# Kernel tuning notes

Measured on AMD Instinct MI355X. Metric: run time of the kernel, lower is better.

The kernel has to match this reference:

```python
import jax, jax.numpy as jnp
import numpy as np

NUM_JOINTS = 24
NUM_THETAS = NUM_JOINTS * 3  # 72
NUM_VERTS = 6890
NUM_BETAS = 10
BATCH = 512

SMPL_PARENTS = np.array([0, 0, 0, 0, 1, 2, 3, 4, 5, 6, 7, 8, 9, 9, 9,
                         12, 13, 14, 16, 17, 18, 19, 20, 21], dtype=np.int32)


def setup_inputs() -> dict:
    key = jax.random.key(0)
    ks = jax.random.split(key, 6)
    x = jax.random.normal(ks[0], (BATCH, NUM_THETAS + NUM_BETAS), dtype=jnp.float32) * 0.3
    v_template = jax.random.normal(ks[1], (NUM_VERTS, 3), dtype=jnp.float32) * 0.3
    shapedirs = jax.random.normal(ks[2], (NUM_BETAS, NUM_VERTS * 3), dtype=jnp.float32) * 0.01
    posedirs = jax.random.normal(ks[3], (207, NUM_VERTS * 3), dtype=jnp.float32) * 0.001
    Jr = jax.random.uniform(ks[4], (NUM_VERTS, NUM_JOINTS), dtype=jnp.float32)
    J_regressor = Jr / jnp.sum(Jr, axis=0, keepdims=True)
    W = jax.random.uniform(ks[5], (NUM_VERTS, NUM_JOINTS), dtype=jnp.float32)
    lbs_weights = W / jnp.sum(W, axis=1, keepdims=True)  # rows sum to 1 (skinning weights)
    parents = jnp.asarray(SMPL_PARENTS)
    return {"x": x, "v_template": v_template, "shapedirs": shapedirs,
            "J_regressor": J_regressor, "posedirs": posedirs,
            "lbs_weights": lbs_weights, "parents": parents}


def batch_rodrigues(theta):
    # theta: [N,3] axis-angle -> [N,3,3] rotation matrices
    angle = jnp.linalg.norm(theta + 1e-8, axis=1, keepdims=True)  # [N,1]
    r = theta / angle                                              # [N,3] unit axis
    cos = jnp.cos(angle)[..., None]                                # [N,1,1]
    sin = jnp.sin(angle)[..., None]
    outer = r[:, :, None] * r[:, None, :]                          # [N,3,3]
    rx, ry, rz = r[:, 0], r[:, 1], r[:, 2]
    zero = jnp.zeros_like(rx)
    K = jnp.stack([zero, -rz, ry,
                   rz, zero, -rx,
                   -ry, rx, zero], axis=1).reshape(-1, 3, 3)       # skew-symmetric
    eye = jnp.eye(3, dtype=theta.dtype)
    return cos * eye + (1.0 - cos) * outer + sin * K


def global_rigid_transformation(Rs, J, parents):
    # Rs: [B,24,3,3], J: [B,24,3] -> A: [B,24,4,4]
    B = Rs.shape[0]
    dtype = Rs.dtype
    bottom = jnp.broadcast_to(jnp.array([0, 0, 0, 1], dtype=dtype), (B, 1, 4))

    def make_A(R, t):  # R:[B,3,3], t:[B,3]
        Rt = jnp.concatenate([R, t[:, :, None]], axis=2)  # [B,3,4]
        return jnp.concatenate([Rt, bottom], axis=1)       # [B,4,4]

    parents = np.asarray(parents)
    results = [make_A(Rs[:, 0], J[:, 0])]
    for i in range(1, NUM_JOINTS):
        t_rel = J[:, i] - J[:, parents[i]]
        A_here = make_A(Rs[:, i], t_rel)
        results.append(jnp.matmul(results[parents[i]], A_here))
    results = jnp.stack(results, axis=1)  # [B,24,4,4]

    Js_w0 = jnp.concatenate([J, jnp.zeros((B, NUM_JOINTS, 1), dtype=dtype)], axis=2)  # [B,24,4]
    init_bone = jnp.einsum('bjpq,bjq->bjp', results, Js_w0)                           # [B,24,4]
    A = results - jnp.pad(init_bone[..., None], ((0, 0), (0, 0), (0, 0), (3, 0)))
    return A


def reference(x, v_template, shapedirs, J_regressor, posedirs, lbs_weights, parents):
    B = x.shape[0]
    thetas = x[:, :NUM_THETAS]
    betas = x[:, NUM_THETAS:]

    # shape blendshapes
    v_shaped = (betas @ shapedirs).reshape(B, NUM_VERTS, 3) + v_template  # [B,V,3]

    J = jnp.einsum('bvc,vj->bjc', v_shaped, J_regressor)  # [B,24,3]

    # pose rotations + pose blendshapes
    Rs = batch_rodrigues(thetas.reshape(-1, 3)).reshape(B, NUM_JOINTS, 3, 3)
    pose_feature = (Rs[:, 1:] - jnp.eye(3, dtype=x.dtype)).reshape(B, 207)
    v_posed = (pose_feature @ posedirs).reshape(B, NUM_VERTS, 3) + v_shaped

    # kinematic chain
    A = global_rigid_transformation(Rs, J, parents)  # [B,24,4,4]

    # linear blend skinning
    T = jnp.einsum('vj,bjpq->bvpq', lbs_weights, A)  # [B,V,4,4]
    v_posed_homo = jnp.concatenate(
        [v_posed, jnp.ones((B, NUM_VERTS, 1), dtype=x.dtype)], axis=2)  # [B,V,4]
    verts = jnp.einsum('bvpq,bvq->bvp', T, v_posed_homo)[:, :, :3]
    return verts
```

## Files before the change

### kernel.cpp

```cpp
#include <hip/hip_runtime.h>

#define NUM_JOINTS 24
#define NUM_VERTS  6890
#define NUM_COORDS (NUM_VERTS * 3)
#define NUM_BETAS  10
#define KTOT       217
#define KPAD       224
#define BATCH      512
#define VPAD       6912

#define WS_SJP  0
#define WS_XBF  85536
#define WS_DBF  142880
#define WS_WHBF 2465312
#define WS_AH   2575904
#define WS_AL   2706976

typedef __attribute__((ext_vector_type(8))) short short8;
typedef __attribute__((ext_vector_type(4))) float f32x4;

__device__ inline unsigned short f2bf(float f) {
    union { float f; unsigned u; } c; c.f = f;
    unsigned u = c.u;
    u += 0x7fffu + ((u >> 16) & 1u);
    return (unsigned short)(u >> 16);
}
__device__ inline float bf2f(unsigned short h) {
    union { unsigned u; float f; } c; c.u = ((unsigned)h) << 16;
    return c.f;
}

struct PBShm {
    float Rs[4][24][9];
    float Jl[4][24][3];
    float Rg[4][24][9];
    float tg[4][24][3];
    float As[4][24][12];
};

__global__ __launch_bounds__(256) void k_prep(const float* __restrict__ Jr,
                                              const float* __restrict__ sd,
                                              const float* __restrict__ pd,
                                              const float* __restrict__ vt,
                                              const float* __restrict__ w,
                                              float* __restrict__ ws) {
    __shared__ __align__(16) unsigned char smem[28928];
    const int t   = blockIdx.x;
    const int tid = threadIdx.x;
    unsigned short* whbf = (unsigned short*)(ws + WS_WHBF);
    unsigned short* dbf  = (unsigned short*)(ws + WS_DBF);

    if (t < 27) {
        const int v = t * 256 + tid;
        const bool ok = (v < NUM_VERTS);
        unsigned short row[32];
        #pragma unroll
        for (int j = 0; j < 32; ++j)
            row[j] = f2bf((ok && j < 24) ? w[v * 24 + j] : 0.f);
        #pragma unroll
        for (int i = 0; i < 4; ++i)
            *(float4*)(whbf + (size_t)v * 32 + i * 8) = *(const float4*)(&row[i * 8]);
    } else if (t < 351) {
        unsigned* L = (unsigned*)smem;
        const int c0   = (t - 27) * 64;
        const int lane = tid & 63;
        const int grp  = tid >> 6;
        const int c    = c0 + lane;
        const bool cv  = (c < NUM_COORDS);
        #pragma unroll 4
        for (int i = 0; i < 28; ++i) {
            const int p  = i * 4 + grp;
            const int k0 = 2 * p, k1 = k0 + 1;
            float v0 = 0.f, v1 = 0.f;
            if (cv) {
                v0 = (k0 < 10) ? sd[(size_t)k0 * NUM_COORDS + c]
                   : (k0 < KTOT) ? pd[(size_t)(k0 - 10) * NUM_COORDS + c] : 0.f;
                v1 = (k1 < 10) ? sd[(size_t)k1 * NUM_COORDS + c]
                   : (k1 < KTOT) ? pd[(size_t)(k1 - 10) * NUM_COORDS + c] : 0.f;
            }
            L[lane * 113 + p] = (unsigned)f2bf(v0) | ((unsigned)f2bf(v1) << 16);
        }
        __syncthreads();
        #pragma unroll
        for (int i = 0; i < 7; ++i) {
            const int idx = i * 256 + tid;
            const int row = idx / 28;
            const int q   = idx % 28;
            uint4 val;
            val.x = L[row * 113 + q * 4 + 0];
            val.y = L[row * 113 + q * 4 + 1];
            val.z = L[row * 113 + q * 4 + 2];
            val.w = L[row * 113 + q * 4 + 3];
            *(uint4*)(dbf + (size_t)(c0 + row) * KPAD + q * 8) = val;
        }
    } else {
        float* Jl = (float*)smem;
        float* S  = (float*)smem + 64 * 25;
        const int strip = t - 351;
        const int v0 = strip * 64;
        #pragma unroll
        for (int i = 0; i < 6; ++i) {
            const int idx = i * 256 + tid;
            const int v = idx / 24, j = idx % 24;
            Jl[v * 25 + j] = (v0 + v < NUM_VERTS) ? Jr[(size_t)(v0 + v) * 24 + j] : 0.f;
        }
        #pragma unroll
        for (int i = 0; i < 9; ++i) {
            const int idx = i * 256 + tid;
            if (idx < 33 * 64) {
                const int s = idx / 64, v = idx % 64;
                float val = 0.f;
                if (v0 + v < NUM_VERTS) {
                    if (s < 30) val = sd[(size_t)(s / 3) * NUM_COORDS + (size_t)(v0 + v) * 3 + (s % 3)];
                    else        val = vt[(size_t)(v0 + v) * 3 + (s - 30)];
                }
                S[s * 64 + v] = val;
            }
        }
        __syncthreads();
        float* wsp = ws + WS_SJP + (size_t)strip * 792;
        for (int o = tid; o < 792; o += 256) {
            const int s = o / 24, j = o % 24;
            float sum = 0.f;
            #pragma unroll 8
            for (int v = 0; v < 64; ++v)
                sum += S[s * 64 + v] * Jl[v * 25 + j];
            wsp[o] = sum;
        }
    }
}

__global__ __launch_bounds__(256) void k_pb(const float* __restrict__ x,
                                            const int* __restrict__ parents,
                                            float* __restrict__ ws) {
    __shared__ PBShm P;
    __shared__ float SJf[792];
    unsigned short* xbf = (unsigned short*)(ws + WS_XBF);
    unsigned short* ahi = (unsigned short*)(ws + WS_AH);
    unsigned short* alo = (unsigned short*)(ws + WS_AL);
    const int tid = threadIdx.x;

    {
        const float* wsp = ws + WS_SJP;
        for (int o = tid; o < 792; o += 256) {
            float sum = 0.f;
            for (int s2 = 0; s2 < 108; ++s2)
                sum += wsp[(size_t)s2 * 792 + o];
            SJf[o] = sum;
        }
    }
    __syncthreads();

    const int sub  = tid >> 6;
    const int lane = tid & 63;
    const int b = blockIdx.x * 4 + sub;
    const float* row = x + b * (NUM_BETAS + 72);

    if (lane < 24) {
        const int j = lane;
        const float t0 = row[3 * j + 0], t1 = row[3 * j + 1], t2 = row[3 * j + 2];
        const float a0 = t0 + 1e-8f, a1 = t1 + 1e-8f, a2 = t2 + 1e-8f;
        const float angle = sqrtf(a0 * a0 + a1 * a1 + a2 * a2);
        const float inv = 1.0f / angle;
        const float rx = t0 * inv, ry = t1 * inv, rz = t2 * inv;
        const float c = cosf(angle), sn = sinf(angle), o = 1.f - c;
        float R[9];
        R[0] = c + o * rx * rx;       R[1] = o * rx * ry - sn * rz; R[2] = o * rx * rz + sn * ry;
        R[3] = o * rx * ry + sn * rz; R[4] = c + o * ry * ry;       R[5] = o * ry * rz - sn * rx;
        R[6] = o * rx * rz - sn * ry; R[7] = o * ry * rz + sn * rx; R[8] = c + o * rz * rz;
        #pragma unroll
        for (int i = 0; i < 9; ++i) P.Rs[sub][j][i] = R[i];
        #pragma unroll
        for (int c3 = 0; c3 < 3; ++c3) {
            float s = SJf[(30 + c3) * 24 + j];
            #pragma unroll
            for (int k = 0; k < NUM_BETAS; ++k)
                s += row[72 + k] * SJf[(k * 3 + c3) * 24 + j];
            P.Jl[sub][j][c3] = s;
        }
        if (j >= 1) {
            #pragma unroll
            for (int i = 0; i < 9; ++i) {
                const float pf = R[i] - ((i == 0 || i == 4 || i == 8) ? 1.f : 0.f);
                xbf[(size_t)b * KPAD + 10 + (j - 1) * 9 + i] = f2bf(pf);
            }
        }
    }
    if (lane < NUM_BETAS) xbf[(size_t)b * KPAD + lane] = f2bf(row[72 + lane]);
    if (lane == 63) {
        #pragma unroll
        for (int k = KTOT; k < KPAD; ++k) xbf[(size_t)b * KPAD + k] = 0;
    }
    __syncthreads();

    if (lane == 0) {
        float Rg[24][9], tg[24][3];
        #pragma unroll
        for (int q = 0; q < 9; ++q) { Rg[0][q] = P.Rs[sub][0][q]; P.Rg[sub][0][q] = Rg[0][q]; }
        #pragma unroll
        for (int c3 = 0; c3 < 3; ++c3) { tg[0][c3] = P.Jl[sub][0][c3]; P.tg[sub][0][c3] = tg[0][c3]; }

        #pragma unroll
        for (int i = 1; i < 24; ++i) {
            constexpr int PAR[24] = {0, 0, 0, 0, 1, 2, 3, 4, 5, 6, 7, 8,
                                     9, 9, 9, 12, 13, 14, 16, 17, 18, 19, 20, 21};
            const int p = PAR[i];
            float Rsl[9];
            #pragma unroll
            for (int q = 0; q < 9; ++q) Rsl[q] = P.Rs[sub][i][q];
            float tmp[9];
            #pragma unroll
            for (int r = 0; r < 3; ++r)
                #pragma unroll
                for (int cc = 0; cc < 3; ++cc)
                    tmp[r * 3 + cc] = Rg[p][r * 3 + 0] * Rsl[0 + cc] +
                                      Rg[p][r * 3 + 1] * Rsl[3 + cc] +
                                      Rg[p][r * 3 + 2] * Rsl[6 + cc];
            #pragma unroll
            for (int q = 0; q < 9; ++q) { Rg[i][q] = tmp[q]; P.Rg[sub][i][q] = tmp[q]; }
            const float tr0 = P.Jl[sub][i][0] - P.Jl[sub][p][0];
            const float tr1 = P.Jl[sub][i][1] - P.Jl[sub][p][1];
            const float tr2 = P.Jl[sub][i][2] - P.Jl[sub][p][2];
            #pragma unroll
            for (int r = 0; r < 3; ++r) {
                tg[i][r] = Rg[p][r * 3 + 0] * tr0 + Rg[p][r * 3 + 1] * tr1 +
                           Rg[p][r * 3 + 2] * tr2 + tg[p][r];
                P.tg[sub][i][r] = tg[i][r];
            }
        }
    }
    __syncthreads();

    if (lane < 24) {
        const int j = lane;
        #pragma unroll
        for (int r = 0; r < 3; ++r) {
            const float tt = P.tg[sub][j][r] - (P.Rg[sub][j][r * 3 + 0] * P.Jl[sub][j][0] +
                                                P.Rg[sub][j][r * 3 + 1] * P.Jl[sub][j][1] +
                                                P.Rg[sub][j][r * 3 + 2] * P.Jl[sub][j][2]);
            P.As[sub][j][r * 4 + 0] = P.Rg[sub][j][r * 3 + 0];
            P.As[sub][j][r * 4 + 1] = P.Rg[sub][j][r * 3 + 1];
            P.As[sub][j][r * 4 + 2] = P.Rg[sub][j][r * 3 + 2];
            P.As[sub][j][r * 4 + 3] = tt;
        }
    }
    __syncthreads();

    if (lane < 32) {
        const int r = lane >> 1;
        const int half = lane & 1;
        unsigned short hi[16], lo[16];
        #pragma unroll
        for (int i = 0; i < 16; ++i) {
            const int j = half * 16 + i;
            float v = 0.f;
            if (r < 12 && j < 24) v = P.As[sub][j][r];
            const unsigned short h = f2bf(v);
            hi[i] = h;
            lo[i] = f2bf(v - bf2f(h));
        }
        unsigned short* dh = ahi + ((size_t)b * 16 + r) * 32 + half * 16;
        unsigned short* dl = alo + ((size_t)b * 16 + r) * 32 + half * 16;
        #pragma unroll
        for (int i = 0; i < 2; ++i) {
            *(float4*)(dh + i * 8) = *(const float4*)(&hi[i * 8]);
            *(float4*)(dl + i * 8) = *(const float4*)(&lo[i * 8]);
        }
    }
}

__global__ __launch_bounds__(256) void k_fused(const float* __restrict__ vt,
                                               float* __restrict__ out,
                                               float* __restrict__ ws) {
    __shared__ __align__(16) float VP[32 * 194];
    __shared__ __align__(16) unsigned char U[20480];
    unsigned short* Xs = (unsigned short*)U;
    float*          Tsf = (float*)U;

    const unsigned short* dbf  = (const unsigned short*)(ws + WS_DBF);
    const unsigned short* xbf  = (const unsigned short*)(ws + WS_XBF);
    const unsigned short* whbf = (const unsigned short*)(ws + WS_WHBF);
    const unsigned short* ahi  = (const unsigned short*)(ws + WS_AH);
    const unsigned short* alo  = (const unsigned short*)(ws + WS_AL);

    const int tid  = threadIdx.x;
    const int wave = tid >> 6;
    const int lane = tid & 63;
    const int col  = lane & 15;
    const int quad = lane >> 4;
    const int c0   = blockIdx.x * 192;
    const int b0   = blockIdx.y * 32;

    short8 bfrag[3][7];
    float vtl[3];
    #pragma unroll
    for (int nt = 0; nt < 3; ++nt) {
        const int nc = c0 + wave * 48 + nt * 16 + col;
        const unsigned short* brow = dbf + (size_t)nc * KPAD + quad * 8;
        #pragma unroll
        for (int kb = 0; kb < 7; ++kb)
            bfrag[nt][kb] = *(const short8*)(brow + kb * 32);
        vtl[nt] = (nc < NUM_COORDS) ? vt[nc] : 0.f;
    }

    #pragma unroll
    for (int i = 0; i < 4; ++i) {
        const int c = tid + i * 256;
        if (c < 32 * 28) {
            const int r = c / 28, off = c % 28;
            *(float4*)(&Xs[r * 232 + off * 8]) =
                *(const float4*)(xbf + (size_t)(b0 + r) * KPAD + off * 8);
        }
    }
    __syncthreads();

    #pragma unroll
    for (int mt = 0; mt < 2; ++mt) {
        const unsigned short* arow = &Xs[(mt * 16 + col) * 232 + quad * 8];
        f32x4 acc[3] = {{0.f,0.f,0.f,0.f},{0.f,0.f,0.f,0.f},{0.f,0.f,0.f,0.f}};
        #pragma unroll
        for (int kb = 0; kb < 7; ++kb) {
            const short8 af = *(const short8*)(arow + kb * 32);
            #pragma unroll
            for (int nt = 0; nt < 3; ++nt)
                acc[nt] = __builtin_amdgcn_mfma_f32_16x16x32_bf16(af, bfrag[nt][kb], acc[nt], 0, 0, 0);
        }
        #pragma unroll
        for (int nt = 0; nt < 3; ++nt) {
            const int cc = wave * 48 + nt * 16 + col;
            #pragma unroll
            for (int r = 0; r < 4; ++r)
                VP[(mt * 16 + quad * 4 + r) * 194 + cc] = acc[nt][r] + vtl[nt];
        }
    }
    __syncthreads();

    const int v0 = blockIdx.x * 64;
    short8 wfrag[4];
    #pragma unroll
    for (int mt = 0; mt < 4; ++mt)
        wfrag[mt] = *(const short8*)(whbf + (size_t)(v0 + mt * 16 + col) * 32 + quad * 8);

    float* ts = Tsf + wave * (64 * 20);
    const int vv = v0 + lane;
    const bool vok = (vv < NUM_VERTS);

    for (int nt = wave; nt < 32; nt += 4) {
        const int b = b0 + nt;
        const short8 bh = *(const short8*)(ahi + ((size_t)b * 16 + col) * 32 + quad * 8);
        const short8 bl = *(const short8*)(alo + ((size_t)b * 16 + col) * 32 + quad * 8);

        f32x4 acc2[4];
        #pragma unroll
        for (int mt = 0; mt < 4; ++mt) {
            f32x4 z = {0.f, 0.f, 0.f, 0.f};
            z = __builtin_amdgcn_mfma_f32_16x16x32_bf16(wfrag[mt], bh, z, 0, 0, 0);
            z = __builtin_amdgcn_mfma_f32_16x16x32_bf16(wfrag[mt], bl, z, 0, 0, 0);
            acc2[mt] = z;
        }
        #pragma unroll
        for (int mt = 0; mt < 4; ++mt)
            #pragma unroll
            for (int r = 0; r < 4; ++r)
                ts[(mt * 16 + quad * 4 + r) * 20 + col] = acc2[mt][r];

        const f32x4 t0 = *(const f32x4*)(ts + lane * 20 + 0);
        const f32x4 t1 = *(const f32x4*)(ts + lane * 20 + 4);
        const f32x4 t2 = *(const f32x4*)(ts + lane * 20 + 8);

        const float h0 = VP[nt * 194 + lane * 3 + 0];
        const float h1 = VP[nt * 194 + lane * 3 + 1];
        const float h2 = VP[nt * 194 + lane * 3 + 2];

        if (vok) {
            float* orow = out + (size_t)b * NUM_COORDS + (size_t)vv * 3;
            __builtin_nontemporal_store(t0[0] * h0 + t0[1] * h1 + t0[2] * h2 + t0[3], orow + 0);
            __builtin_nontemporal_store(t1[0] * h0 + t1[1] * h1 + t1[2] * h2 + t1[3], orow + 1);
            __builtin_nontemporal_store(t2[0] * h0 + t2[1] * h1 + t2[2] * h2 + t2[3], orow + 2);
        }
    }
}

extern "C" void kernel_launch(void* const* d_in, const int* in_sizes, int n_in,
                              void* d_out, int out_size, void* d_ws, size_t ws_size,
                              hipStream_t stream) {
    const float* x  = (const float*)d_in[0];
    const float* vt = (const float*)d_in[1];
    const float* sd = (const float*)d_in[2];
    const float* Jr = (const float*)d_in[3];
    const float* pd = (const float*)d_in[4];
    const float* w  = (const float*)d_in[5];
    const int* parents = (const int*)d_in[6];
    float* out = (float*)d_out;
    float* ws  = (float*)d_ws;

    k_prep <<<459, 256, 0, stream>>>(Jr, sd, pd, vt, w, ws);
    k_pb   <<<128, 256, 0, stream>>>(x, parents, ws);
    k_fused<<<dim3(108, 16), 256, 0, stream>>>(vt, out, ws);
}
```

Baseline: 153.9 us.

## Cut LDS and register footprint of fused skinning kernel to raise occupancy

Removes the shared-memory staging of the batch-feature tile and the preloaded 21 B-fragment registers. The first GEMM now streams A and B fragments straight from global memory per k-block. The per-wave transform scratch is halved by writing the skinning result in two 32-vertex halves, and launch bounds request 4 blocks per SM. This lowers LDS and VGPR usage to fit more blocks per CU, at the cost of redundant global fragment loads across waves and an extra serialized write/read phase in the output loop.

```diff
diff --git a/kernel.cpp b/kernel.cpp
--- a/kernel.cpp
+++ b/kernel.cpp
@@ -269,13 +269,11 @@
     }
 }
 
-__global__ __launch_bounds__(256) void k_fused(const float* __restrict__ vt,
-                                               float* __restrict__ out,
-                                               float* __restrict__ ws) {
+__global__ __launch_bounds__(256, 4) void k_fused(const float* __restrict__ vt,
+                                                  float* __restrict__ out,
+                                                  float* __restrict__ ws) {
     __shared__ __align__(16) float VP[32 * 194];
-    __shared__ __align__(16) unsigned char U[20480];
-    unsigned short* Xs = (unsigned short*)U;
-    float*          Tsf = (float*)U;
+    __shared__ __align__(16) float Tsf[4][32 * 20];
 
     const unsigned short* dbf  = (const unsigned short*)(ws + WS_DBF);
     const unsigned short* xbf  = (const unsigned short*)(ws + WS_XBF);
@@ -291,48 +289,42 @@
     const int c0   = blockIdx.x * 192;
     const int b0   = blockIdx.y * 32;
 
-    short8 bfrag[3][7];
     float vtl[3];
     #pragma unroll
     for (int nt = 0; nt < 3; ++nt) {
         const int nc = c0 + wave * 48 + nt * 16 + col;
-        const unsigned short* brow = dbf + (size_t)nc * KPAD + quad * 8;
-        #pragma unroll
-        for (int kb = 0; kb < 7; ++kb)
-            bfrag[nt][kb] = *(const short8*)(brow + kb * 32);
         vtl[nt] = (nc < NUM_COORDS) ? vt[nc] : 0.f;
     }
 
+    f32x4 acc[2][3] = {{{0.f,0.f,0.f,0.f},{0.f,0.f,0.f,0.f},{0.f,0.f,0.f,0.f}},
+                       {{0.f,0.f,0.f,0.f},{0.f,0.f,0.f,0.f},{0.f,0.f,0.f,0.f}}};
     #pragma unroll
-    for (int i = 0; i < 4; ++i) {
-        const int c = tid + i * 256;
-        if (c < 32 * 28) {
-            const int r = c / 28, off = c % 28;
-            *(float4*)(&Xs[r * 232 + off * 8]) =
-                *(const float4*)(xbf + (size_t)(b0 + r) * KPAD + off * 8);
-        }
-    }
-    __syncthreads();
-
+    for (int kb = 0; kb < 7; ++kb) {
+        short8 b3[3];
+        #pragma unroll
+        for (int nt = 0; nt < 3; ++nt) {
+            const int nc = c0 + wave * 48 + nt * 16 + col;
+            b3[nt] = *(const short8*)(dbf + (size_t)nc * KPAD + quad * 8 + kb * 32);
+        }
+        short8 a2[2];
+        #pragma unroll
+        for (int mt = 0; mt < 2; ++mt)
+            a2[mt] = *(const short8*)(xbf + (size_t)(b0 + mt * 16 + col) * KPAD + quad * 8 + kb * 32);
+        #pragma unroll
+        for (int mt = 0; mt < 2; ++mt)
+            #pragma unroll
+            for (int nt = 0; nt < 3; ++nt)
+                acc[mt][nt] = __builtin_amdgcn_mfma_f32_16x16x32_bf16(a2[mt], b3[nt], acc[mt][nt], 0, 0, 0);
+    }
     #pragma unroll
-    for (int mt = 0; mt < 2; ++mt) {
-        const unsigned short* arow = &Xs[(mt * 16 + col) * 232 + quad * 8];
-        f32x4 acc[3] = {{0.f,0.f,0.f,0.f},{0.f,0.f,0.f,0.f},{0.f,0.f,0.f,0.f}};
-        #pragma unroll
-        for (int kb = 0; kb < 7; ++kb) {
-            const short8 af = *(const short8*)(arow + kb * 32);
-            #pragma unroll
-            for (int nt = 0; nt < 3; ++nt)
-                acc[nt] = __builtin_amdgcn_mfma_f32_16x16x32_bf16(af, bfrag[nt][kb], acc[nt], 0, 0, 0);
-        }
+    for (int mt = 0; mt < 2; ++mt)
         #pragma unroll
         for (int nt = 0; nt < 3; ++nt) {
             const int cc = wave * 48 + nt * 16 + col;
             #pragma unroll
             for (int r = 0; r < 4; ++r)
-                VP[(mt * 16 + quad * 4 + r) * 194 + cc] = acc[nt][r] + vtl[nt];
-        }
-    }
+                VP[(mt * 16 + quad * 4 + r) * 194 + cc] = acc[mt][nt][r] + vtl[nt];
+        }
     __syncthreads();
 
     const int v0 = blockIdx.x * 64;
@@ -341,9 +333,10 @@
     for (int mt = 0; mt < 4; ++mt)
         wfrag[mt] = *(const short8*)(whbf + (size_t)(v0 + mt * 16 + col) * 32 + quad * 8);
 
-    float* ts = Tsf + wave * (64 * 20);
+    float* ts = &Tsf[wave][0];
     const int vv = v0 + lane;
     const bool vok = (vv < NUM_VERTS);
+    const int lhalf = lane & 31;
 
     for (int nt = wave; nt < 32; nt += 4) {
         const int b = b0 + nt;
@@ -358,25 +351,41 @@
             z = __builtin_amdgcn_mfma_f32_16x16x32_bf16(wfrag[mt], bl, z, 0, 0, 0);
             acc2[mt] = z;
         }
-        #pragma unroll
-        for (int mt = 0; mt < 4; ++mt)
-            #pragma unroll
-            for (int r = 0; r < 4; ++r)
-                ts[(mt * 16 + quad * 4 + r) * 20 + col] = acc2[mt][r];
-
-        const f32x4 t0 = *(const f32x4*)(ts + lane * 20 + 0);
-        const f32x4 t1 = *(const f32x4*)(ts + lane * 20 + 4);
-        const f32x4 t2 = *(const f32x4*)(ts + lane * 20 + 8);
 
         const float h0 = VP[nt * 194 + lane * 3 + 0];
         const float h1 = VP[nt * 194 + lane * 3 + 1];
         const float h2 = VP[nt * 194 + lane * 3 + 2];
-
-        if (vok) {
-            float* orow = out + (size_t)b * NUM_COORDS + (size_t)vv * 3;
-            __builtin_nontemporal_store(t0[0] * h0 + t0[1] * h1 + t0[2] * h2 + t0[3], orow + 0);
-            __builtin_nontemporal_store(t1[0] * h0 + t1[1] * h1 + t1[2] * h2 + t1[3], orow + 1);
-            __builtin_nontemporal_store(t2[0] * h0 + t2[1] * h1 + t2[2] * h2 + t2[3], orow + 2);
+        float* orow = out + (size_t)b * NUM_COORDS + (size_t)vv * 3;
+
+        #pragma unroll
+        for (int mt = 0; mt < 2; ++mt)
+            #pragma unroll
+            for (int r = 0; r < 4; ++r)
+                ts[(mt * 16 + quad * 4 + r) * 20 + col] = acc2[mt][r];
+        if (lane < 32) {
+            const f32x4 t0 = *(const f32x4*)(ts + lhalf * 20 + 0);
+            const f32x4 t1 = *(const f32x4*)(ts + lhalf * 20 + 4);
+            const f32x4 t2 = *(const f32x4*)(ts + lhalf * 20 + 8);
+            if (vok) {
+                __builtin_nontemporal_store(t0[0] * h0 + t0[1] * h1 + t0[2] * h2 + t0[3], orow + 0);
+                __builtin_nontemporal_store(t1[0] * h0 + t1[1] * h1 + t1[2] * h2 + t1[3], orow + 1);
+                __builtin_nontemporal_store(t2[0] * h0 + t2[1] * h1 + t2[2] * h2 + t2[3], orow + 2);
+            }
+        }
+        #pragma unroll
+        for (int mt = 2; mt < 4; ++mt)
+            #pragma unroll
+            for (int r = 0; r < 4; ++r)
+                ts[((mt - 2) * 16 + quad * 4 + r) * 20 + col] = acc2[mt][r];
+        if (lane >= 32) {
+            const f32x4 t0 = *(const f32x4*)(ts + lhalf * 20 + 0);
+            const f32x4 t1 = *(const f32x4*)(ts + lhalf * 20 + 4);
+            const f32x4 t2 = *(const f32x4*)(ts + lhalf * 20 + 8);
+            if (vok) {
+                __builtin_nontemporal_store(t0[0] * h0 + t0[1] * h1 + t0[2] * h2 + t0[3], orow + 0);
+                __builtin_nontemporal_store(t1[0] * h0 + t1[1] * h1 + t1[2] * h2 + t1[3], orow + 1);
+                __builtin_nontemporal_store(t2[0] * h0 + t2[1] * h1 + t2[2] * h2 + t2[3], orow + 2);
+            }
         }
     }
 }
```

Measured after the change: 154.5 us. Within noise of the previous version (+0.4%).
